# Kernel tuning notes

Hardware: AMD Instinct MI355X
Metric: run time of the kernel (lower is better)

The kernel has to match this reference:

```python
import jax, jax.numpy as jnp
import numpy as np

MASK_PENALTY = 10000.0

def setup_inputs() -> dict:
    key = jax.random.key(0)
    kq, kk, kv = jax.random.split(key, 3)
    B, S, D = 8, 2048, 64
    return {
        "query": jax.random.normal(kq, (B, S, D), dtype=jnp.float32),
        "key": jax.random.normal(kk, (B, S, D), dtype=jnp.float32),
        "value": jax.random.normal(kv, (B, S, D), dtype=jnp.float32),
        "mask": jnp.ones((B, S), dtype=jnp.bool_),
    }

def reference(query, key, value, mask):
    # e: [B, Sq, Sk]
    d = query.shape[-1]
    e = jnp.einsum('bqd,bkd->bqk', query, key) / jnp.sqrt(jnp.float32(d))
    Sq, Sk = query.shape[1], key.shape[1]
    # history_only causal mask: key index > query index gets -10000
    causal = (jnp.arange(Sk)[None, :] > jnp.arange(Sq)[:, None]).astype(jnp.float32)
    e = e - MASK_PENALTY * causal[None, :, :]
    # padding mask: [B, Sk] -> [B, 1, Sk]
    e = e - MASK_PENALTY * (1.0 - mask.astype(jnp.float32))[:, None, :]
    attn = jax.nn.softmax(e, axis=-1)
    return jnp.einsum('bqk,bkd->bqd', attn, value)
```

## Files before the change

### kernel.cpp

```cpp
#include <hip/hip_runtime.h>


typedef _Float16 f16x8 __attribute__((ext_vector_type(8)));
typedef _Float16 f16x4 __attribute__((ext_vector_type(4)));
typedef float    f32x4 __attribute__((ext_vector_type(4)));

#define MFMA_K32(A, B, C) __builtin_amdgcn_mfma_f32_16x16x32_f16(A, B, C, 0, 0, 0)
#define MFMA_K16(A, B, C) __builtin_amdgcn_mfma_f32_16x16x16f16(A, B, C, 0, 0, 0)

__device__ inline unsigned pack2h(float a, float b) {
    union { _Float16 h[2]; unsigned u; } t;
    t.h[0] = (_Float16)a; t.h[1] = (_Float16)b;
    return t.u;
}

__global__ __launch_bounds__(256, 4)
void prep_f16(const float* __restrict__ K, const float* __restrict__ V,
              _Float16* __restrict__ Kh, _Float16* __restrict__ Vq) {
    __shared__ _Float16 sT[64 * 80];
    const int b   = blockIdx.x >> 5;
    const int s0  = (blockIdx.x & 31) * 64;
    const int t   = threadIdx.x;
    const int row = t >> 2;
    const int grp = (t & 3) * 16;
    const size_t base = ((size_t)b * 2048 + s0 + row) * 64 + grp;
    {
        union { _Float16 h[16]; f16x8 v[2]; } o;
        const float* p = K + base;
#pragma unroll
        for (int i = 0; i < 16; i += 4) {
            float4 x = *(const float4*)(p + i);
            o.h[i] = (_Float16)x.x; o.h[i+1] = (_Float16)x.y;
            o.h[i+2] = (_Float16)x.z; o.h[i+3] = (_Float16)x.w;
        }
        *(f16x8*)(Kh + base) = o.v[0];
        *(f16x8*)(Kh + base + 8) = o.v[1];
    }
    {
        const float* p = V + base;
#pragma unroll
        for (int i = 0; i < 16; i += 4) {
            float4 x = *(const float4*)(p + i);
            sT[(grp + i    ) * 80 + row] = (_Float16)x.x;
            sT[(grp + i + 1) * 80 + row] = (_Float16)x.y;
            sT[(grp + i + 2) * 80 + row] = (_Float16)x.z;
            sT[(grp + i + 3) * 80 + row] = (_Float16)x.w;
        }
    }
    __syncthreads();
    {
        const int d = t & 63, g = t >> 6;
        const size_t o = (((size_t)b * 128 + (s0 >> 4) + g) * 64 + d) * 16;
        *(f16x8*)(Vq + o)     = *(const f16x8*)&sT[d * 80 + g * 16];
        *(f16x8*)(Vq + o + 8) = *(const f16x8*)&sT[d * 80 + g * 16 + 8];
    }
}

__global__ __launch_bounds__(512, 4)
void attn_f16_v4(const float* __restrict__ Q, const _Float16* __restrict__ Kh,
                 const _Float16* __restrict__ Vq, const int* __restrict__ M,
                 float* __restrict__ O) {
    constexpr int S = 2048, D = 64;
    constexpr float CSCALE = 0.18033688011112042f;

    __shared__ float sO[8][16 * 64];
    __shared__ float sL[8][16];

    const int tid  = threadIdx.x;
    const int w    = tid >> 6;
    const int lane = tid & 63;
    const int l15  = lane & 15;
    const int quad = lane >> 4;

    for (int phase = 0; phase < 2; ++phase) {
        const int batch = (int)blockIdx.y ^ phase;
        const int tile  = phase ? 127 - (int)blockIdx.x : (int)blockIdx.x;
        const int n_kt  = tile / 2 + 1;
        const int qg0   = tile * 16;
        const size_t bq = (size_t)batch * S;
        const _Float16* Kb = Kh + bq * D;
        const _Float16* Vb = Vq + bq * D;

        f16x8 qf[2];
        {
            const float* qp = Q + (bq + qg0 + l15) * D + quad * 8;
#pragma unroll
            for (int dc = 0; dc < 2; ++dc) {
                float4 x0 = *(const float4*)(qp + dc * 32);
                float4 x1 = *(const float4*)(qp + dc * 32 + 4);
                union { unsigned u[4]; f16x8 v; } t;
                t.u[0] = pack2h(x0.x, x0.y); t.u[1] = pack2h(x0.z, x0.w);
                t.u[2] = pack2h(x1.x, x1.y); t.u[3] = pack2h(x1.z, x1.w);
                qf[dc] = t.v;
            }
        }

        f32x4 acc[4];
        float lacc = 0.f;
#pragma unroll
        for (int c = 0; c < 4; ++c) { acc[c][0] = acc[c][1] = acc[c][2] = acc[c][3] = 0.f; }

        f16x8 kn[2][2]; f16x4 vn[2][4]; int4 mn[2];
        if (w < n_kt) {
            const int kb = w * 32;
#pragma unroll
            for (int kg = 0; kg < 2; ++kg)
#pragma unroll
                for (int dc = 0; dc < 2; ++dc)
                    kn[kg][dc] = *(const f16x8*)(Kb + (size_t)(kb + kg * 16 + l15) * D + dc * 32 + quad * 8);
#pragma unroll
            for (int kg = 0; kg < 2; ++kg)
#pragma unroll
                for (int c = 0; c < 4; ++c)
                    vn[kg][c] = *(const f16x4*)(Vb + ((size_t)((kb >> 4) + kg) * 64 + c * 16 + l15) * 16 + quad * 4);
            mn[0] = *(const int4*)(M + bq + kb + quad * 4);
            mn[1] = *(const int4*)(M + bq + kb + 16 + quad * 4);
        }

        for (int t = w; t < n_kt; t += 8) {
            const int kb = t * 32;
            f16x8 k00 = kn[0][0], k01 = kn[0][1], k10 = kn[1][0], k11 = kn[1][1];
            f16x4 v00 = vn[0][0], v01 = vn[0][1], v02 = vn[0][2], v03 = vn[0][3];
            f16x4 v10 = vn[1][0], v11 = vn[1][1], v12 = vn[1][2], v13 = vn[1][3];
            union { int a[4]; int4 v; } m0, m1;
            m0.v = mn[0]; m1.v = mn[1];
            if (t + 8 < n_kt) {
                const int kb2 = kb + 256;
#pragma unroll
                for (int kg = 0; kg < 2; ++kg)
#pragma unroll
                    for (int dc = 0; dc < 2; ++dc)
                        kn[kg][dc] = *(const f16x8*)(Kb + (size_t)(kb2 + kg * 16 + l15) * D + dc * 32 + quad * 8);
#pragma unroll
                for (int kg = 0; kg < 2; ++kg)
#pragma unroll
                    for (int c = 0; c < 4; ++c)
                        vn[kg][c] = *(const f16x4*)(Vb + ((size_t)((kb2 >> 4) + kg) * 64 + c * 16 + l15) * 16 + quad * 4);
                mn[0] = *(const int4*)(M + bq + kb2 + quad * 4);
                mn[1] = *(const int4*)(M + bq + kb2 + 16 + quad * 4);
            }

            f32x4 scT0, scT1;
            {
                f32x4 z; z[0] = z[1] = z[2] = z[3] = 0.f;
                f32x4 y0 = MFMA_K32(k00, qf[0], z);
                scT0 = MFMA_K32(k01, qf[1], y0);
                f32x4 y1 = MFMA_K32(k10, qf[0], z);
                scT1 = MFMA_K32(k11, qf[1], y1);
            }

            f16x4 pf0, pf1;
            {
                union { _Float16 h[4]; f16x4 v; } pp;
#pragma unroll
                for (int r = 0; r < 4; ++r) {
                    const int key = kb + quad * 4 + r;
                    float e  = __builtin_amdgcn_exp2f(scT0[r] * CSCALE);
                    bool  ok = (key <= qg0 + l15) && (m0.a[r] != 0);
                    float pv = ok ? e : 0.f;
                    lacc += pv;
                    pp.h[r] = (_Float16)pv;
                }
                pf0 = pp.v;
#pragma unroll
                for (int r = 0; r < 4; ++r) {
                    const int key = kb + 16 + quad * 4 + r;
                    float e  = __builtin_amdgcn_exp2f(scT1[r] * CSCALE);
                    bool  ok = (key <= qg0 + l15) && (m1.a[r] != 0);
                    float pv = ok ? e : 0.f;
                    lacc += pv;
                    pp.h[r] = (_Float16)pv;
                }
                pf1 = pp.v;
            }

            acc[0] = MFMA_K16(pf0, v00, acc[0]);
            acc[1] = MFMA_K16(pf0, v01, acc[1]);
            acc[2] = MFMA_K16(pf0, v02, acc[2]);
            acc[3] = MFMA_K16(pf0, v03, acc[3]);
            acc[0] = MFMA_K16(pf1, v10, acc[0]);
            acc[1] = MFMA_K16(pf1, v11, acc[1]);
            acc[2] = MFMA_K16(pf1, v12, acc[2]);
            acc[3] = MFMA_K16(pf1, v13, acc[3]);
        }

        lacc += __shfl_xor(lacc, 16, 64);
        lacc += __shfl_xor(lacc, 32, 64);

#pragma unroll
        for (int c = 0; c < 4; ++c)
#pragma unroll
            for (int r = 0; r < 4; ++r)
                sO[w][(quad * 4 + r) * 64 + c * 16 + l15] = acc[c][r];
        if (lane < 16) sL[w][l15] = lacc;
        __syncthreads();
        {
            const int row = tid >> 5;
            const int col = (tid & 31) * 2;
            float a = 0.f, b = 0.f, l = 0.f;
#pragma unroll
            for (int w2 = 0; w2 < 8; ++w2) {
                a += sO[w2][row * 64 + col];
                b += sO[w2][row * 64 + col + 1];
                l += sL[w2][row];
            }
            const float inv = 1.f / fmaxf(l, 1e-37f);
            float2 o; o.x = a * inv; o.y = b * inv;
            *(float2*)(&O[(bq + qg0 + row) * D + col]) = o;
        }
        __syncthreads();
    }
}

constexpr int PSTR = 40;
__global__ __launch_bounds__(512, 4)
void attn_f16_slow(const float* __restrict__ Q, const float* __restrict__ K,
                   const float* __restrict__ V, const int* __restrict__ M,
                   float* __restrict__ O) {
    constexpr int S = 2048, D = 64;
    constexpr float CSCALE = 0.18033688011112042f;
    __shared__ __align__(16) _Float16 sP[8][16 * PSTR];
    __shared__ float sO[8][16 * 64];
    __shared__ float sL[8][16];
    const int tid = threadIdx.x, w = tid >> 6, lane = tid & 63;
    const int l15 = lane & 15, quad = lane >> 4;
    for (int phase = 0; phase < 2; ++phase) {
        const int batch = (int)blockIdx.y ^ phase;
        const int tile  = phase ? 127 - (int)blockIdx.x : (int)blockIdx.x;
        const int n_kt  = tile / 2 + 1;
        const int qg0   = tile * 16;
        const size_t bq = (size_t)batch * S;
        f16x8 qf[2];
        {
            const float* qp = Q + (bq + qg0 + l15) * D + quad * 8;
#pragma unroll
            for (int dc = 0; dc < 2; ++dc) {
                float4 x0 = *(const float4*)(qp + dc * 32);
                float4 x1 = *(const float4*)(qp + dc * 32 + 4);
                union { unsigned u[4]; f16x8 v; } t;
                t.u[0] = pack2h(x0.x, x0.y); t.u[1] = pack2h(x0.z, x0.w);
                t.u[2] = pack2h(x1.x, x1.y); t.u[3] = pack2h(x1.z, x1.w);
                qf[dc] = t.v;
            }
        }
        f32x4 acc[4]; float lacc[4];
#pragma unroll
        for (int c = 0; c < 4; ++c) { acc[c][0] = acc[c][1] = acc[c][2] = acc[c][3] = 0.f; }
#pragma unroll
        for (int r = 0; r < 4; ++r) lacc[r] = 0.f;
        for (int t = w; t < n_kt; t += 8) {
            const int kb = t * 32;
            f16x8 kf[2][2];
            {
                const float* kp = K + (bq + kb + l15) * D + quad * 8;
#pragma unroll
                for (int kg = 0; kg < 2; ++kg)
#pragma unroll
                    for (int dc = 0; dc < 2; ++dc) {
                        float4 x0 = *(const float4*)(kp + kg * 16 * D + dc * 32);
                        float4 x1 = *(const float4*)(kp + kg * 16 * D + dc * 32 + 4);
                        union { unsigned u[4]; f16x8 v; } tt;
                        tt.u[0] = pack2h(x0.x, x0.y); tt.u[1] = pack2h(x0.z, x0.w);
                        tt.u[2] = pack2h(x1.x, x1.y); tt.u[3] = pack2h(x1.z, x1.w);
                        kf[kg][dc] = tt.v;
                    }
            }
            float vr[4][8];
            {
                const float* vp = V + (bq + kb + quad * 8) * D + l15;
#pragma unroll
                for (int c = 0; c < 4; ++c)
#pragma unroll
                    for (int j = 0; j < 8; ++j)
                        vr[c][j] = vp[j * D + c * 16];
            }
            const int m0 = M[bq + kb + l15];
            const int m1 = M[bq + kb + 16 + l15];
            f32x4 sc[2];
#pragma unroll
            for (int kg = 0; kg < 2; ++kg) {
                f32x4 z; z[0] = z[1] = z[2] = z[3] = 0.f;
                z = MFMA_K32(qf[0], kf[kg][0], z);
                sc[kg] = MFMA_K32(qf[1], kf[kg][1], z);
            }
            float p[2][4];
#pragma unroll
            for (int kg = 0; kg < 2; ++kg) {
                const int key = kb + kg * 16 + l15;
                const int mv  = kg ? m1 : m0;
#pragma unroll
                for (int r = 0; r < 4; ++r) {
                    const int qrow = qg0 + quad * 4 + r;
                    float e  = __builtin_amdgcn_exp2f(sc[kg][r] * CSCALE);
                    bool  ok = (key <= qrow) && (mv != 0);
                    float pv = ok ? e : 0.f;
                    p[kg][r] = pv;
                    lacc[r] += pv;
                }
            }
            _Float16* sPw = sP[w];
#pragma unroll
            for (int kg = 0; kg < 2; ++kg)
#pragma unroll
                for (int r = 0; r < 4; ++r)
                    sPw[(quad * 4 + r) * PSTR + kg * 16 + l15] = (_Float16)p[kg][r];
            f16x8 pf = *(const f16x8*)(&sPw[l15 * PSTR + quad * 8]);
#pragma unroll
            for (int c = 0; c < 4; ++c) {
                union { unsigned u[4]; f16x8 v; } tt;
                tt.u[0] = pack2h(vr[c][0], vr[c][1]);
                tt.u[1] = pack2h(vr[c][2], vr[c][3]);
                tt.u[2] = pack2h(vr[c][4], vr[c][5]);
                tt.u[3] = pack2h(vr[c][6], vr[c][7]);
                acc[c] = MFMA_K32(pf, tt.v, acc[c]);
            }
        }
#pragma unroll
        for (int r = 0; r < 4; ++r) {
            float s = lacc[r];
            s += __shfl_xor(s, 1, 64);
            s += __shfl_xor(s, 2, 64);
            s += __shfl_xor(s, 4, 64);
            s += __shfl_xor(s, 8, 64);
            lacc[r] = s;
        }
#pragma unroll
        for (int c = 0; c < 4; ++c)
#pragma unroll
            for (int r = 0; r < 4; ++r)
                sO[w][(quad * 4 + r) * 64 + c * 16 + l15] = acc[c][r];
        if (l15 == 0) {
#pragma unroll
            for (int r = 0; r < 4; ++r) sL[w][quad * 4 + r] = lacc[r];
        }
        __syncthreads();
        {
            const int row = tid >> 5;
            const int col = (tid & 31) * 2;
            float a = 0.f, b = 0.f, l = 0.f;
#pragma unroll
            for (int w2 = 0; w2 < 8; ++w2) {
                a += sO[w2][row * 64 + col];
                b += sO[w2][row * 64 + col + 1];
                l += sL[w2][row];
            }
            const float inv = 1.f / fmaxf(l, 1e-37f);
            float2 o; o.x = a * inv; o.y = b * inv;
            *(float2*)(&O[(bq + qg0 + row) * D + col]) = o;
        }
        __syncthreads();
    }
}

extern "C" void kernel_launch(void* const* d_in, const int* in_sizes, int n_in,
                              void* d_out, int out_size, void* d_ws, size_t ws_size,
                              hipStream_t stream) {
    const float* Q = (const float*)d_in[0];
    const float* K = (const float*)d_in[1];
    const float* V = (const float*)d_in[2];
    const int*   M = (const int*)d_in[3];
    float*       O = (float*)d_out;
    const size_t n_kv = (size_t)8 * 2048 * 64;
    const size_t need = n_kv * 2 * sizeof(_Float16);
    if (ws_size >= need) {
        _Float16* Kh = (_Float16*)d_ws;
        _Float16* Vq = Kh + n_kv;
        hipLaunchKernelGGL(prep_f16, dim3(256), dim3(256), 0, stream, K, V, Kh, Vq);
        hipLaunchKernelGGL(attn_f16_v4, dim3(64, 8), dim3(512), 0, stream, Q, Kh, Vq, M, O);
    } else {
        hipLaunchKernelGGL(attn_f16_slow, dim3(64, 8), dim3(512), 0, stream, Q, K, V, M, O);
    }
}
```

Measured before the change: 98.76 us.

## Process 32-query tiles per block so K/V fragments serve two query groups

Each block now handles one 32-row query tile (two 16-row fragments) instead of two 16-row tiles in separate phases. Every loaded K/V fragment feeds MFMAs for both query fragments, halving K/V global traffic per query. Blocks are ordered heaviest-first to even out the causal load. The softmax scale is folded into K during the f16 prep so the per-score multiply before exp2 goes away, and the output reduction uses a padded shared stride with float4 stores. The cost is more registers per thread and less phase-based balancing across blocks.

```diff
diff --git a/kernel.cpp b/kernel.cpp
--- a/kernel.cpp
+++ b/kernel.cpp
@@ -13,6 +13,8 @@
     t.h[0] = (_Float16)a; t.h[1] = (_Float16)b;
     return t.u;
 }
+
+constexpr float CSCALE = 0.18033688011112042f;
 
 __global__ __launch_bounds__(256, 4)
 void prep_f16(const float* __restrict__ K, const float* __restrict__ V,
@@ -30,8 +32,8 @@
 #pragma unroll
         for (int i = 0; i < 16; i += 4) {
             float4 x = *(const float4*)(p + i);
-            o.h[i] = (_Float16)x.x; o.h[i+1] = (_Float16)x.y;
-            o.h[i+2] = (_Float16)x.z; o.h[i+3] = (_Float16)x.w;
+            o.h[i]   = (_Float16)(x.x * CSCALE); o.h[i+1] = (_Float16)(x.y * CSCALE);
+            o.h[i+2] = (_Float16)(x.z * CSCALE); o.h[i+3] = (_Float16)(x.w * CSCALE);
         }
         *(f16x8*)(Kh + base) = o.v[0];
         *(f16x8*)(Kh + base + 8) = o.v[1];
@@ -56,15 +58,16 @@
     }
 }
 
+constexpr int SOSTR = 68;
+
 __global__ __launch_bounds__(512, 4)
-void attn_f16_v4(const float* __restrict__ Q, const _Float16* __restrict__ Kh,
+void attn_f16_v5(const float* __restrict__ Q, const _Float16* __restrict__ Kh,
                  const _Float16* __restrict__ Vq, const int* __restrict__ M,
                  float* __restrict__ O) {
     constexpr int S = 2048, D = 64;
-    constexpr float CSCALE = 0.18033688011112042f;
-
-    __shared__ float sO[8][16 * 64];
-    __shared__ float sL[8][16];
+
+    __shared__ float sO[8][32 * SOSTR];
+    __shared__ float sL[8][32];
 
     const int tid  = threadIdx.x;
     const int w    = tid >> 6;
@@ -72,143 +75,150 @@
     const int l15  = lane & 15;
     const int quad = lane >> 4;
 
-    for (int phase = 0; phase < 2; ++phase) {
-        const int batch = (int)blockIdx.y ^ phase;
-        const int tile  = phase ? 127 - (int)blockIdx.x : (int)blockIdx.x;
-        const int n_kt  = tile / 2 + 1;
-        const int qg0   = tile * 16;
-        const size_t bq = (size_t)batch * S;
-        const _Float16* Kb = Kh + bq * D;
-        const _Float16* Vb = Vq + bq * D;
-
-        f16x8 qf[2];
-        {
-            const float* qp = Q + (bq + qg0 + l15) * D + quad * 8;
-#pragma unroll
-            for (int dc = 0; dc < 2; ++dc) {
-                float4 x0 = *(const float4*)(qp + dc * 32);
-                float4 x1 = *(const float4*)(qp + dc * 32 + 4);
-                union { unsigned u[4]; f16x8 v; } t;
-                t.u[0] = pack2h(x0.x, x0.y); t.u[1] = pack2h(x0.z, x0.w);
-                t.u[2] = pack2h(x1.x, x1.y); t.u[3] = pack2h(x1.z, x1.w);
-                qf[dc] = t.v;
-            }
-        }
-
-        f32x4 acc[4];
-        float lacc = 0.f;
-#pragma unroll
-        for (int c = 0; c < 4; ++c) { acc[c][0] = acc[c][1] = acc[c][2] = acc[c][3] = 0.f; }
-
-        f16x8 kn[2][2]; f16x4 vn[2][4]; int4 mn[2];
-        if (w < n_kt) {
-            const int kb = w * 32;
+    const int st    = 63 - (int)blockIdx.x;
+    const int batch = (int)blockIdx.y;
+    const int n_kt  = st + 1;
+    const int qg0   = st * 32;
+    const size_t bq = (size_t)batch * S;
+    const _Float16* Kb = Kh + bq * D;
+    const _Float16* Vb = Vq + bq * D;
+
+    f16x8 qf[2][2];
+#pragma unroll
+    for (int f = 0; f < 2; ++f) {
+        const float* qp = Q + (bq + qg0 + f * 16 + l15) * D + quad * 8;
+#pragma unroll
+        for (int dc = 0; dc < 2; ++dc) {
+            float4 x0 = *(const float4*)(qp + dc * 32);
+            float4 x1 = *(const float4*)(qp + dc * 32 + 4);
+            union { unsigned u[4]; f16x8 v; } t;
+            t.u[0] = pack2h(x0.x, x0.y); t.u[1] = pack2h(x0.z, x0.w);
+            t.u[2] = pack2h(x1.x, x1.y); t.u[3] = pack2h(x1.z, x1.w);
+            qf[f][dc] = t.v;
+        }
+    }
+
+    f32x4 acc[2][4];
+    float lacc[2] = {0.f, 0.f};
+#pragma unroll
+    for (int f = 0; f < 2; ++f)
+#pragma unroll
+        for (int c = 0; c < 4; ++c) { acc[f][c][0] = acc[f][c][1] = acc[f][c][2] = acc[f][c][3] = 0.f; }
+
+    f16x8 kn[2][2]; f16x4 vn[2][4]; int4 mn[2];
+    if (w < n_kt) {
+        const int kb = w * 32;
+#pragma unroll
+        for (int kg = 0; kg < 2; ++kg)
+#pragma unroll
+            for (int dc = 0; dc < 2; ++dc)
+                kn[kg][dc] = *(const f16x8*)(Kb + (size_t)(kb + kg * 16 + l15) * D + dc * 32 + quad * 8);
+#pragma unroll
+        for (int kg = 0; kg < 2; ++kg)
+#pragma unroll
+            for (int c = 0; c < 4; ++c)
+                vn[kg][c] = *(const f16x4*)(Vb + ((size_t)((kb >> 4) + kg) * 64 + c * 16 + l15) * 16 + quad * 4);
+        mn[0] = *(const int4*)(M + bq + kb + quad * 4);
+        mn[1] = *(const int4*)(M + bq + kb + 16 + quad * 4);
+    }
+
+    for (int t = w; t < n_kt; t += 8) {
+        const int kb = t * 32;
+        f16x8 k00 = kn[0][0], k01 = kn[0][1], k10 = kn[1][0], k11 = kn[1][1];
+        f16x4 v00 = vn[0][0], v01 = vn[0][1], v02 = vn[0][2], v03 = vn[0][3];
+        f16x4 v10 = vn[1][0], v11 = vn[1][1], v12 = vn[1][2], v13 = vn[1][3];
+        union { int a[4]; int4 v; } m0, m1;
+        m0.v = mn[0]; m1.v = mn[1];
+        if (t + 8 < n_kt) {
+            const int kb2 = kb + 256;
 #pragma unroll
             for (int kg = 0; kg < 2; ++kg)
 #pragma unroll
                 for (int dc = 0; dc < 2; ++dc)
-                    kn[kg][dc] = *(const f16x8*)(Kb + (size_t)(kb + kg * 16 + l15) * D + dc * 32 + quad * 8);
+                    kn[kg][dc] = *(const f16x8*)(Kb + (size_t)(kb2 + kg * 16 + l15) * D + dc * 32 + quad * 8);
 #pragma unroll
             for (int kg = 0; kg < 2; ++kg)
 #pragma unroll
                 for (int c = 0; c < 4; ++c)
-                    vn[kg][c] = *(const f16x4*)(Vb + ((size_t)((kb >> 4) + kg) * 64 + c * 16 + l15) * 16 + quad * 4);
-            mn[0] = *(const int4*)(M + bq + kb + quad * 4);
-            mn[1] = *(const int4*)(M + bq + kb + 16 + quad * 4);
-        }
-
-        for (int t = w; t < n_kt; t += 8) {
-            const int kb = t * 32;
-            f16x8 k00 = kn[0][0], k01 = kn[0][1], k10 = kn[1][0], k11 = kn[1][1];
-            f16x4 v00 = vn[0][0], v01 = vn[0][1], v02 = vn[0][2], v03 = vn[0][3];
-            f16x4 v10 = vn[1][0], v11 = vn[1][1], v12 = vn[1][2], v13 = vn[1][3];
-            union { int a[4]; int4 v; } m0, m1;
-            m0.v = mn[0]; m1.v = mn[1];
-            if (t + 8 < n_kt) {
-                const int kb2 = kb + 256;
-#pragma unroll
-                for (int kg = 0; kg < 2; ++kg)
-#pragma unroll
-                    for (int dc = 0; dc < 2; ++dc)
-                        kn[kg][dc] = *(const f16x8*)(Kb + (size_t)(kb2 + kg * 16 + l15) * D + dc * 32 + quad * 8);
-#pragma unroll
-                for (int kg = 0; kg < 2; ++kg)
-#pragma unroll
-                    for (int c = 0; c < 4; ++c)
-                        vn[kg][c] = *(const f16x4*)(Vb + ((size_t)((kb2 >> 4) + kg) * 64 + c * 16 + l15) * 16 + quad * 4);
-                mn[0] = *(const int4*)(M + bq + kb2 + quad * 4);
-                mn[1] = *(const int4*)(M + bq + kb2 + 16 + quad * 4);
-            }
-
+                    vn[kg][c] = *(const f16x4*)(Vb + ((size_t)((kb2 >> 4) + kg) * 64 + c * 16 + l15) * 16 + quad * 4);
+            mn[0] = *(const int4*)(M + bq + kb2 + quad * 4);
+            mn[1] = *(const int4*)(M + bq + kb2 + 16 + quad * 4);
+        }
+
+#pragma unroll
+        for (int f = 0; f < 2; ++f) {
             f32x4 scT0, scT1;
             {
                 f32x4 z; z[0] = z[1] = z[2] = z[3] = 0.f;
-                f32x4 y0 = MFMA_K32(k00, qf[0], z);
-                scT0 = MFMA_K32(k01, qf[1], y0);
-                f32x4 y1 = MFMA_K32(k10, qf[0], z);
-                scT1 = MFMA_K32(k11, qf[1], y1);
-            }
-
+                f32x4 y0 = MFMA_K32(k00, qf[f][0], z);
+                scT0 = MFMA_K32(k01, qf[f][1], y0);
+                f32x4 y1 = MFMA_K32(k10, qf[f][0], z);
+                scT1 = MFMA_K32(k11, qf[f][1], y1);
+            }
+            const int qrow = qg0 + f * 16 + l15;
             f16x4 pf0, pf1;
             {
                 union { _Float16 h[4]; f16x4 v; } pp;
 #pragma unroll
                 for (int r = 0; r < 4; ++r) {
                     const int key = kb + quad * 4 + r;
-                    float e  = __builtin_amdgcn_exp2f(scT0[r] * CSCALE);
-                    bool  ok = (key <= qg0 + l15) && (m0.a[r] != 0);
+                    float e  = __builtin_amdgcn_exp2f(scT0[r]);
+                    bool  ok = (key <= qrow) && (m0.a[r] != 0);
                     float pv = ok ? e : 0.f;
-                    lacc += pv;
+                    lacc[f] += pv;
                     pp.h[r] = (_Float16)pv;
                 }
                 pf0 = pp.v;
 #pragma unroll
                 for (int r = 0; r < 4; ++r) {
                     const int key = kb + 16 + quad * 4 + r;
-                    float e  = __builtin_amdgcn_exp2f(scT1[r] * CSCALE);
-                    bool  ok = (key <= qg0 + l15) && (m1.a[r] != 0);
+                    float e  = __builtin_amdgcn_exp2f(scT1[r]);
+                    bool  ok = (key <= qrow) && (m1.a[r] != 0);
                     float pv = ok ? e : 0.f;
-                    lacc += pv;
+                    lacc[f] += pv;
                     pp.h[r] = (_Float16)pv;
                 }
                 pf1 = pp.v;
             }
-
-            acc[0] = MFMA_K16(pf0, v00, acc[0]);
-            acc[1] = MFMA_K16(pf0, v01, acc[1]);
-            acc[2] = MFMA_K16(pf0, v02, acc[2]);
-            acc[3] = MFMA_K16(pf0, v03, acc[3]);
-            acc[0] = MFMA_K16(pf1, v10, acc[0]);
-            acc[1] = MFMA_K16(pf1, v11, acc[1]);
-            acc[2] = MFMA_K16(pf1, v12, acc[2]);
-            acc[3] = MFMA_K16(pf1, v13, acc[3]);
-        }
-
-        lacc += __shfl_xor(lacc, 16, 64);
-        lacc += __shfl_xor(lacc, 32, 64);
-
+            acc[f][0] = MFMA_K16(pf0, v00, acc[f][0]);
+            acc[f][1] = MFMA_K16(pf0, v01, acc[f][1]);
+            acc[f][2] = MFMA_K16(pf0, v02, acc[f][2]);
+            acc[f][3] = MFMA_K16(pf0, v03, acc[f][3]);
+            acc[f][0] = MFMA_K16(pf1, v10, acc[f][0]);
+            acc[f][1] = MFMA_K16(pf1, v11, acc[f][1]);
+            acc[f][2] = MFMA_K16(pf1, v12, acc[f][2]);
+            acc[f][3] = MFMA_K16(pf1, v13, acc[f][3]);
+        }
+    }
+
+#pragma unroll
+    for (int f = 0; f < 2; ++f) {
+        lacc[f] += __shfl_xor(lacc[f], 16, 64);
+        lacc[f] += __shfl_xor(lacc[f], 32, 64);
+    }
+
+#pragma unroll
+    for (int f = 0; f < 2; ++f)
 #pragma unroll
         for (int c = 0; c < 4; ++c)
 #pragma unroll
             for (int r = 0; r < 4; ++r)
-                sO[w][(quad * 4 + r) * 64 + c * 16 + l15] = acc[c][r];
-        if (lane < 16) sL[w][l15] = lacc;
-        __syncthreads();
-        {
-            const int row = tid >> 5;
-            const int col = (tid & 31) * 2;
-            float a = 0.f, b = 0.f, l = 0.f;
-#pragma unroll
-            for (int w2 = 0; w2 < 8; ++w2) {
-                a += sO[w2][row * 64 + col];
-                b += sO[w2][row * 64 + col + 1];
-                l += sL[w2][row];
-            }
-            const float inv = 1.f / fmaxf(l, 1e-37f);
-            float2 o; o.x = a * inv; o.y = b * inv;
-            *(float2*)(&O[(bq + qg0 + row) * D + col]) = o;
-        }
-        __syncthreads();
+                sO[w][(f * 16 + quad * 4 + r) * SOSTR + c * 16 + l15] = acc[f][c][r];
+    if (lane < 16) { sL[w][l15] = lacc[0]; sL[w][16 + l15] = lacc[1]; }
+    __syncthreads();
+    {
+        const int row = tid >> 4;
+        const int col = (tid & 15) * 4;
+        float a0 = 0.f, a1 = 0.f, a2 = 0.f, a3 = 0.f, l = 0.f;
+#pragma unroll
+        for (int w2 = 0; w2 < 8; ++w2) {
+            const float* p = &sO[w2][row * SOSTR + col];
+            a0 += p[0]; a1 += p[1]; a2 += p[2]; a3 += p[3];
+            l  += sL[w2][row];
+        }
+        const float inv = 1.f / fmaxf(l, 1e-37f);
+        float4 o; o.x = a0 * inv; o.y = a1 * inv; o.z = a2 * inv; o.w = a3 * inv;
+        *(float4*)(&O[(bq + qg0 + row) * D + col]) = o;
     }
 }
 
@@ -218,7 +228,6 @@
                    const float* __restrict__ V, const int* __restrict__ M,
                    float* __restrict__ O) {
     constexpr int S = 2048, D = 64;
-    constexpr float CSCALE = 0.18033688011112042f;
     __shared__ __align__(16) _Float16 sP[8][16 * PSTR];
     __shared__ float sO[8][16 * 64];
     __shared__ float sL[8][16];
@@ -260,8 +269,10 @@
                         float4 x0 = *(const float4*)(kp + kg * 16 * D + dc * 32);
                         float4 x1 = *(const float4*)(kp + kg * 16 * D + dc * 32 + 4);
                         union { unsigned u[4]; f16x8 v; } tt;
-                        tt.u[0] = pack2h(x0.x, x0.y); tt.u[1] = pack2h(x0.z, x0.w);
-                        tt.u[2] = pack2h(x1.x, x1.y); tt.u[3] = pack2h(x1.z, x1.w);
+                        tt.u[0] = pack2h(x0.x * CSCALE, x0.y * CSCALE);
+                        tt.u[1] = pack2h(x0.z * CSCALE, x0.w * CSCALE);
+                        tt.u[2] = pack2h(x1.x * CSCALE, x1.y * CSCALE);
+                        tt.u[3] = pack2h(x1.z * CSCALE, x1.w * CSCALE);
                         kf[kg][dc] = tt.v;
                     }
             }
@@ -291,7 +302,7 @@
 #pragma unroll
                 for (int r = 0; r < 4; ++r) {
                     const int qrow = qg0 + quad * 4 + r;
-                    float e  = __builtin_amdgcn_exp2f(sc[kg][r] * CSCALE);
+                    float e  = __builtin_amdgcn_exp2f(sc[kg][r]);
                     bool  ok = (key <= qrow) && (mv != 0);
                     float pv = ok ? e : 0.f;
                     p[kg][r] = pv;
@@ -366,7 +377,7 @@
         _Float16* Kh = (_Float16*)d_ws;
         _Float16* Vq = Kh + n_kv;
         hipLaunchKernelGGL(prep_f16, dim3(256), dim3(256), 0, stream, K, V, Kh, Vq);
-        hipLaunchKernelGGL(attn_f16_v4, dim3(64, 8), dim3(512), 0, stream, Q, Kh, Vq, M, O);
+        hipLaunchKernelGGL(attn_f16_v5, dim3(64, 8), dim3(512), 0, stream, Q, Kh, Vq, M, O);
     } else {
         hipLaunchKernelGGL(attn_f16_slow, dim3(64, 8), dim3(512), 0, stream, Q, K, V, M, O);
     }
```

Result: slower. 140.9 us (+42.7%).
